# Performance work log

Measured on AMD Instinct MI355X. Metric: run time of the kernel, lower is better.

## Reference

```python
import jax, jax.numpy as jnp
import numpy as np

D_IN = 1024
D_OUT = 1024
N_HEADS = 16
HEAD_DIM = D_IN // N_HEADS      # 64
HEAD_DIM_V = D_OUT // N_HEADS   # 64


def setup_inputs() -> dict:
    key = jax.random.key(0)
    ks = jax.random.split(key, 7)
    s = 0.02
    x = jax.random.normal(ks[0], (4, 2048, D_IN), dtype=jnp.float32)
    Wq = jax.random.normal(ks[1], (D_IN, D_IN), dtype=jnp.float32) * s
    bq = jnp.zeros((D_IN,), dtype=jnp.float32)
    Wk = jax.random.normal(ks[2], (D_IN, D_IN), dtype=jnp.float32) * s
    bk = jnp.zeros((D_IN,), dtype=jnp.float32)
    Wv = jax.random.normal(ks[3], (D_IN, D_OUT), dtype=jnp.float32) * s
    bv = jnp.zeros((D_OUT,), dtype=jnp.float32)
    return {"x": x, "Wq": Wq, "bq": bq, "Wk": Wk, "bk": bk, "Wv": Wv, "bv": bv}


def reference(x, Wq, bq, Wk, bk, Wv, bv):
    B, S, _ = x.shape
    scale = jnp.sqrt(jnp.asarray(HEAD_DIM, dtype=jnp.float32))
    # projections -> [B, S, H, Dh] -> [B, H, S, Dh]
    q = (x @ Wq + bq).reshape(B, S, N_HEADS, HEAD_DIM).transpose(0, 2, 1, 3)
    k = (x @ Wk + bk).reshape(B, S, N_HEADS, HEAD_DIM).transpose(0, 2, 1, 3)
    v = (x @ Wv + bv).reshape(B, S, N_HEADS, HEAD_DIM_V).transpose(0, 2, 1, 3)
    # [B, H, S, S] attention scores (naive full materialization, as in source)
    scores = jnp.einsum("bhsd,bhtd->bhst", q, k) / scale
    weights = jax.nn.softmax(scores, axis=-1)
    out = jnp.einsum("bhst,bhtd->bhsd", weights, v)
    # [B, H, S, Dv] -> [B, S, H*Dv]  (out_projection NOT applied in source forward)
    return out.transpose(0, 2, 1, 3).reshape(B, S, N_HEADS * HEAD_DIM_V)
```

## Files before the change

### kernel.cpp

```cpp
#include <hip/hip_runtime.h>

#define B_  4
#define S_  2048
#define D_  1024
#define H_  16
#define DH_ 64
#define M_  (B_ * S_)

typedef __attribute__((ext_vector_type(8))) short short8;
typedef __attribute__((ext_vector_type(4))) float floatx4;

__device__ __forceinline__ unsigned short f2bf(float f) {
    union { float f; unsigned int i; } v; v.f = f;
    unsigned int r = v.i + 0x7fffu + ((v.i >> 16) & 1u);
    return (unsigned short)(r >> 16);
}
__device__ __forceinline__ unsigned int pk_trunc(float a, float b) {
#if __has_builtin(__builtin_amdgcn_perm)
    return __builtin_amdgcn_perm(__float_as_uint(b), __float_as_uint(a), 0x07060302u);
#else
    return (__float_as_uint(a) >> 16) | (__float_as_uint(b) & 0xffff0000u);
#endif
}

#if __has_builtin(__builtin_amdgcn_exp2f)
#define EXP2(x) __builtin_amdgcn_exp2f(x)
#else
#define EXP2(x) __expf(0.6931471805599453f * (x))
#endif

typedef const __attribute__((address_space(1))) unsigned int* gas_ptr;
typedef __attribute__((address_space(3))) unsigned int* las_ptr;
__device__ __forceinline__ void async_cp16(const void* g, void* l) {
    __builtin_amdgcn_global_load_lds((gas_ptr)g, (las_ptr)l, 16, 0, 0);
}

#define VMC3 asm volatile("s_waitcnt vmcnt(3)" ::: "memory")
#define VMC0 asm volatile("s_waitcnt vmcnt(0)" ::: "memory")

__global__ __launch_bounds__(256) void cast_fused_kernel(
    const float* __restrict__ x, unsigned short* __restrict__ Ax,
    const float* __restrict__ W0, const float* __restrict__ W1,
    const float* __restrict__ W2,
    unsigned short* __restrict__ T0, unsigned short* __restrict__ T1,
    unsigned short* __restrict__ T2)
{
    const int bid = blockIdx.x;
    const int t = threadIdx.x;
    if (bid < 8192) {
        int i4 = bid * 256 + t;
        float4 v = reinterpret_cast<const float4*>(x)[i4];
        ushort4 o;
        o.x = f2bf(v.x); o.y = f2bf(v.y); o.z = f2bf(v.z); o.w = f2bf(v.w);
        reinterpret_cast<ushort4*>(Ax)[i4] = o;
        return;
    }
    const int idx = bid - 8192;
    const int z   = idx >> 8;
    const int rem = idx & 255;
    const float* W = z == 0 ? W0 : (z == 1 ? W1 : W2);
    unsigned short* Wt = z == 0 ? T0 : (z == 1 ? T1 : T2);

    __shared__ unsigned short T[64][72];
    const int k0 = (rem & 15) * 64, n0 = (rem >> 4) * 64;

    #pragma unroll
    for (int p = 0; p < 4; ++p) {
        int kr = p * 16 + (t >> 4);
        int nc = (t & 15) * 4;
        float4 v = *reinterpret_cast<const float4*>(W + (size_t)(k0 + kr) * D_ + n0 + nc);
        T[nc + 0][kr] = f2bf(v.x);
        T[nc + 1][kr] = f2bf(v.y);
        T[nc + 2][kr] = f2bf(v.z);
        T[nc + 3][kr] = f2bf(v.w);
    }
    __syncthreads();

    const int nl = t >> 2, kc = (t & 3) * 16;
    size_t base = (size_t)(n0 + nl) * D_ + k0 + kc;
    *reinterpret_cast<short8*>(Wt + base)     = *reinterpret_cast<const short8*>(&T[nl][kc]);
    *reinterpret_cast<short8*>(Wt + base + 8) = *reinterpret_cast<const short8*>(&T[nl][kc + 8]);
}

__global__ __launch_bounds__(512) void gemm_qkv_mfma(
    const unsigned short* __restrict__ Ax,
    const unsigned short* __restrict__ Wt,
    const float* __restrict__ bq, const float* __restrict__ bk,
    const float* __restrict__ bv,
    unsigned short* __restrict__ Q,
    unsigned short* __restrict__ Vtg)
{
    __shared__ unsigned short lds[49152];

    const int tid  = threadIdx.x;
    const int lane = tid & 63;
    const int w    = tid >> 6;
    const int wm   = w >> 2;
    const int wn   = w & 3;
    const int l15  = lane & 15, quad = lane >> 4;

    const int pl   = tid >> 3;
    const int sl   = tid & 7;
    const int xx   = sl ^ (pl & 7);
    const int sro  = pl * 2 + (xx >> 2);
    const int sc   = (xx & 3) * 8;
    const int ldst = tid * 8;
    const int fb = (l15 >> 1) * 64 + ((((l15 & 1) << 2) | quad) ^ (l15 >> 1)) * 8;

    const int id  = blockIdx.x;
    const int g   = (id & 7) * 96 + (id >> 3);
    const int nb  = g >> 6;
    const int mb  = g & 63;
    const int m0  = mb * 128;
    const int n0g = nb * 256;
    const int mat = nb >> 2;
    const int n0m = (nb & 3) * 256;
    const float* bias = mat == 0 ? bq : (mat == 1 ? bk : bv);

    #define ASTG(kcol, reg) \
        async_cp16(Ax + (size_t)(m0 + sro) * 1024 + (kcol) + sc, lds + (reg) + ldst)
    #define BSTG(kcol, reg) do { \
        async_cp16(Wt + (size_t)(n0g + sro) * 1024 + (kcol) + sc,       lds + (reg) + ldst); \
        async_cp16(Wt + (size_t)(n0g + 128 + sro) * 1024 + (kcol) + sc, lds + (reg) + 4096 + ldst); \
    } while (0)

    floatx4 acc[4][4] = {};

    ASTG(0, 0);      BSTG(0, 8192);
    ASTG(32, 4096);  BSTG(32, 16384);
    ASTG(64, 24576); BSTG(64, 32768);
    VMC3;
    __builtin_amdgcn_s_barrier();

    #define PH(bufS, ksub, STAGE_STMT, WAIT_STMT) do { \
        short8 af[4], bfr[4]; \
        _Pragma("unroll") \
        for (int i = 0; i < 4; ++i) \
            af[i] = *reinterpret_cast<const short8*>(lds + (bufS) + (ksub) * 4096 + wm * 2048 + i * 512 + fb); \
        _Pragma("unroll") \
        for (int j = 0; j < 4; ++j) \
            bfr[j] = *reinterpret_cast<const short8*>(lds + (bufS) + 8192 + (ksub) * 8192 + wn * 2048 + j * 512 + fb); \
        STAGE_STMT; \
        __builtin_amdgcn_s_barrier(); \
        asm volatile("s_waitcnt lgkmcnt(0)" ::: "memory"); \
        __builtin_amdgcn_sched_barrier(0); \
        __builtin_amdgcn_s_setprio(1); \
        _Pragma("unroll") \
        for (int i = 0; i < 4; ++i) \
            _Pragma("unroll") \
            for (int j = 0; j < 4; ++j) \
                acc[i][j] = __builtin_amdgcn_mfma_f32_16x16x32_bf16(af[i], bfr[j], acc[i][j], 0, 0, 0); \
        __builtin_amdgcn_s_setprio(0); \
        WAIT_STMT; \
        __builtin_amdgcn_s_barrier(); \
    } while (0)

    #pragma unroll 1
    for (int it = 0; it < 8; ++it) {
        const bool nl = (it < 7);
        const int  kA = (2 * it + 1) * 64;
        const int  kB = kA + 64;
        const int  kC = kA + 128;
        PH(0,     0, { ASTG(kA + 32, 28672); BSTG(kA + 32, 40960); }, );
        PH(0,     1, if (nl) { ASTG(kB, 0); BSTG(kB, 8192); }, { if (nl) VMC3; else VMC0; });
        PH(24576, 0, if (nl) { ASTG(kB + 32, 4096); BSTG(kB + 32, 16384); }, );
        PH(24576, 1, if (nl) { ASTG(kC, 24576); BSTG(kC, 32768); }, { if (nl) VMC3; });
    }

    float bb[4];
    #pragma unroll
    for (int j = 0; j < 4; ++j) bb[j] = bias[n0m + wn * 64 + j * 16 + l15];

    if (mat == 2) {
        const int bI    = m0 >> 11;
        #pragma unroll
        for (int i = 0; i < 4; ++i) {
            int srow = (m0 & 2047) + wm * 64 + i * 16 + quad * 4;
            #pragma unroll
            for (int j = 0; j < 4; ++j) {
                int col = n0m + wn * 64 + j * 16 + l15;
                ushort4 o;
                o.x = f2bf(acc[i][j][0] + bb[j]);
                o.y = f2bf(acc[i][j][1] + bb[j]);
                o.z = f2bf(acc[i][j][2] + bb[j]);
                o.w = f2bf(acc[i][j][3] + bb[j]);
                *reinterpret_cast<ushort4*>(Vtg + (size_t)(bI * 1024 + col) * S_ + srow) = o;
            }
        }
    } else {
        unsigned short* C = Q + (size_t)mat * M_ * D_;
        const float scq = (mat == 0) ? 0.18033688011112042f : 1.0f;
        #pragma unroll
        for (int i = 0; i < 4; ++i)
            #pragma unroll
            for (int r = 0; r < 4; ++r) {
                int row = m0 + wm * 64 + i * 16 + quad * 4 + r;
                #pragma unroll
                for (int j = 0; j < 4; ++j)
                    C[(size_t)row * D_ + n0m + wn * 64 + j * 16 + l15] = f2bf((acc[i][j][r] + bb[j]) * scq);
            }
    }
}

#define KT_   64
#define NT_   (S_ / KT_)
#define PITCH 72

__global__ __launch_bounds__(256, 4) void attn_mfma(
    const unsigned short* __restrict__ Qg,
    const unsigned short* __restrict__ Kg,
    const unsigned short* __restrict__ Vtg,
    float* __restrict__ out)
{
    __shared__ unsigned short Ks[KT_ * PITCH];
    __shared__ unsigned short Vt[DH_ * PITCH];

    const int tid  = threadIdx.x;
    const int wq   = tid >> 6;
    const int lane = tid & 63;
    const int l15  = lane & 15;
    const int quad = lane >> 4;

    const int id  = blockIdx.x;
    const int bh  = (id & 7) * 8 + ((id >> 3) & 7);
    const int qt  = id >> 6;
    const int b   = bh >> 4;
    const int colbase = (bh & 15) * DH_;
    const int rowQ0 = b * S_ + qt * 128;

    short8 qf[2][2];
    #pragma unroll
    for (int g = 0; g < 2; ++g) {
        int qrow = rowQ0 + wq * 32 + g * 16 + l15;
        qf[g][0] = *reinterpret_cast<const short8*>(Qg + (size_t)qrow * D_ + colbase + quad * 8);
        qf[g][1] = *reinterpret_cast<const short8*>(Qg + (size_t)qrow * D_ + colbase + 32 + quad * 8);
    }

    short8 vones;
    #pragma unroll
    for (int i = 0; i < 8; ++i) vones[i] = (short)0x3F80;

    floatx4 Oacc[2][4] = {};
    floatx4 Lacc[2] = {};

    const int srow = tid >> 3;
    const int sc8  = (tid & 7) * 8;
    const int vc  = sc8 >> 4;
    const int vqk = (sc8 >> 2) & 3;
    const int vk0 = ((vc & 1) << 2) + ((vc >> 1) << 5) + (vqk << 3);

    const unsigned short* Kbase = Kg + (size_t)(b * S_) * D_ + colbase;
    const unsigned short* Vbase = Vtg + (size_t)(bh * 64) * S_;

    short8 kpre[2], vpre[2];
    #pragma unroll
    for (int p = 0; p < 2; ++p) {
        kpre[p] = *reinterpret_cast<const short8*>(Kbase + (size_t)(p * 32 + srow) * D_ + sc8);
        vpre[p] = *reinterpret_cast<const short8*>(Vbase + (size_t)(p * 32 + srow) * S_ + sc8);
    }

    for (int kt = 0; kt < NT_; ++kt) {
        __syncthreads();
        #pragma unroll
        for (int p = 0; p < 2; ++p) {
            *reinterpret_cast<short8*>(&Ks[(p * 32 + srow) * PITCH + sc8]) = kpre[p];
            uint4 u = __builtin_bit_cast(uint4, vpre[p]);
            uint2 lo, hi;
            lo.x = u.x; lo.y = u.y; hi.x = u.z; hi.y = u.w;
            *reinterpret_cast<uint2*>(&Vt[(p * 32 + srow) * PITCH + vk0])     = lo;
            *reinterpret_cast<uint2*>(&Vt[(p * 32 + srow) * PITCH + vk0 + 8]) = hi;
        }
        __syncthreads();
        if (kt + 1 < NT_) {
            int off = (kt + 1) * KT_;
            #pragma unroll
            for (int p = 0; p < 2; ++p) {
                kpre[p] = *reinterpret_cast<const short8*>(Kbase + (size_t)(off + p * 32 + srow) * D_ + sc8);
                vpre[p] = *reinterpret_cast<const short8*>(Vbase + (size_t)(p * 32 + srow) * S_ + off + sc8);
            }
        }

        #pragma unroll
        for (int half = 0; half < 2; ++half) {
            floatx4 s_[2][2];
            __builtin_amdgcn_s_setprio(1);
            #pragma unroll
            for (int ci = 0; ci < 2; ++ci) {
                int c = half * 2 + ci;
                short8 kf0 = *reinterpret_cast<const short8*>(&Ks[(c * 16 + l15) * PITCH + quad * 8]);
                short8 kf1 = *reinterpret_cast<const short8*>(&Ks[(c * 16 + l15) * PITCH + 32 + quad * 8]);
                #pragma unroll
                for (int g = 0; g < 2; ++g) {
                    floatx4 a = {0.f, 0.f, 0.f, 0.f};
                    a = __builtin_amdgcn_mfma_f32_16x16x32_bf16(kf0, qf[g][0], a, 0, 0, 0);
                    a = __builtin_amdgcn_mfma_f32_16x16x32_bf16(kf1, qf[g][1], a, 0, 0, 0);
                    s_[g][ci] = a;
                }
            }
            __builtin_amdgcn_s_setprio(0);
            short8 pa[2];
            #pragma unroll
            for (int g = 0; g < 2; ++g) {
                float p00 = EXP2(s_[g][0][0]), p01 = EXP2(s_[g][0][1]);
                float p02 = EXP2(s_[g][0][2]), p03 = EXP2(s_[g][0][3]);
                float p10 = EXP2(s_[g][1][0]), p11 = EXP2(s_[g][1][1]);
                float p12 = EXP2(s_[g][1][2]), p13 = EXP2(s_[g][1][3]);
                uint4 pu;
                pu.x = pk_trunc(p00, p01);
                pu.y = pk_trunc(p02, p03);
                pu.z = pk_trunc(p10, p11);
                pu.w = pk_trunc(p12, p13);
                pa[g] = __builtin_bit_cast(short8, pu);
            }
            __builtin_amdgcn_s_setprio(1);
            #pragma unroll
            for (int g = 0; g < 2; ++g)
                Lacc[g] = __builtin_amdgcn_mfma_f32_16x16x32_bf16(pa[g], vones, Lacc[g], 0, 0, 0);
            #pragma unroll
            for (int d = 0; d < 4; ++d) {
                short8 vf = *reinterpret_cast<const short8*>(
                    &Vt[(d * 16 + l15) * PITCH + half * 32 + quad * 8]);
                #pragma unroll
                for (int g = 0; g < 2; ++g)
                    Oacc[g][d] = __builtin_amdgcn_mfma_f32_16x16x32_bf16(pa[g], vf, Oacc[g][d], 0, 0, 0);
            }
            __builtin_amdgcn_s_setprio(0);
        }
    }

    #pragma unroll
    for (int g = 0; g < 2; ++g) {
        int orow = rowQ0 + wq * 32 + g * 16 + quad * 4;
        #pragma unroll
        for (int r = 0; r < 4; ++r) {
            float inv = 1.f / Lacc[g][r];
            #pragma unroll
            for (int d = 0; d < 4; ++d)
                out[(size_t)(orow + r) * D_ + colbase + d * 16 + l15] = Oacc[g][d][r] * inv;
        }
    }
}

extern "C" void kernel_launch(void* const* d_in, const int* in_sizes, int n_in,
                              void* d_out, int out_size, void* d_ws, size_t ws_size,
                              hipStream_t stream) {
    const float* x  = (const float*)d_in[0];
    const float* Wq = (const float*)d_in[1];
    const float* bq = (const float*)d_in[2];
    const float* Wk = (const float*)d_in[3];
    const float* bk = (const float*)d_in[4];
    const float* Wv = (const float*)d_in[5];
    const float* bv = (const float*)d_in[6];
    float* out = (float*)d_out;

    unsigned short* Q   = (unsigned short*)d_ws;
    unsigned short* K   = Q + (size_t)M_ * D_;
    unsigned short* Vtg = K + (size_t)M_ * D_;
    unsigned short* Ax  = Vtg + (size_t)M_ * D_;
    unsigned short* Wtq = Ax + (size_t)M_ * D_;
    unsigned short* Wtk = Wtq + (size_t)D_ * D_;
    unsigned short* Wtv = Wtk + (size_t)D_ * D_;

    cast_fused_kernel<<<8192 + 768, 256, 0, stream>>>(x, Ax, Wq, Wk, Wv, Wtq, Wtk, Wtv);

    gemm_qkv_mfma<<<768, 512, 0, stream>>>(Ax, Wtq, bq, bk, bv, Q, Vtg);

    attn_mfma<<<1024, 256, 0, stream>>>(Q, K, Vtg, out);
}
```

Before: 232.1 us.

## Double-buffer K/V shared-memory tiles in attention kernel

Splits the K and V shared-memory tiles into two buffers so the next tile is written to LDS while the current one is consumed, with global loads prefetched two tiles ahead. This cuts the two barriers per iteration to one and lets LDS stores overlap the MFMA compute. It doubles LDS use per block (about 36 KB), which may lower occupancy under launch_bounds(256,4), and it keeps the prefetch registers live across the whole loop body.

```diff
diff --git a/kernel.cpp b/kernel.cpp
--- a/kernel.cpp
+++ b/kernel.cpp
@@ -212,8 +212,8 @@
     const unsigned short* __restrict__ Vtg,
     float* __restrict__ out)
 {
-    __shared__ unsigned short Ks[KT_ * PITCH];
-    __shared__ unsigned short Vt[DH_ * PITCH];
+    __shared__ unsigned short Ks[2][KT_ * PITCH];
+    __shared__ unsigned short Vt[2][DH_ * PITCH];
 
     const int tid  = threadIdx.x;
     const int wq   = tid >> 6;
@@ -258,25 +258,46 @@
         kpre[p] = *reinterpret_cast<const short8*>(Kbase + (size_t)(p * 32 + srow) * D_ + sc8);
         vpre[p] = *reinterpret_cast<const short8*>(Vbase + (size_t)(p * 32 + srow) * S_ + sc8);
     }
+    #pragma unroll
+    for (int p = 0; p < 2; ++p) {
+        *reinterpret_cast<short8*>(&Ks[0][(p * 32 + srow) * PITCH + sc8]) = kpre[p];
+        uint4 u = __builtin_bit_cast(uint4, vpre[p]);
+        uint2 lo, hi;
+        lo.x = u.x; lo.y = u.y; hi.x = u.z; hi.y = u.w;
+        *reinterpret_cast<uint2*>(&Vt[0][(p * 32 + srow) * PITCH + vk0])     = lo;
+        *reinterpret_cast<uint2*>(&Vt[0][(p * 32 + srow) * PITCH + vk0 + 8]) = hi;
+    }
+    #pragma unroll
+    for (int p = 0; p < 2; ++p) {
+        kpre[p] = *reinterpret_cast<const short8*>(Kbase + (size_t)(KT_ + p * 32 + srow) * D_ + sc8);
+        vpre[p] = *reinterpret_cast<const short8*>(Vbase + (size_t)(p * 32 + srow) * S_ + KT_ + sc8);
+    }
+    __syncthreads();
 
     for (int kt = 0; kt < NT_; ++kt) {
-        __syncthreads();
-        #pragma unroll
-        for (int p = 0; p < 2; ++p) {
-            *reinterpret_cast<short8*>(&Ks[(p * 32 + srow) * PITCH + sc8]) = kpre[p];
-            uint4 u = __builtin_bit_cast(uint4, vpre[p]);
-            uint2 lo, hi;
-            lo.x = u.x; lo.y = u.y; hi.x = u.z; hi.y = u.w;
-            *reinterpret_cast<uint2*>(&Vt[(p * 32 + srow) * PITCH + vk0])     = lo;
-            *reinterpret_cast<uint2*>(&Vt[(p * 32 + srow) * PITCH + vk0 + 8]) = hi;
-        }
-        __syncthreads();
+        const int cur = kt & 1;
+        const unsigned short* Kc = &Ks[cur][0];
+        const unsigned short* Vc = &Vt[cur][0];
+
         if (kt + 1 < NT_) {
-            int off = (kt + 1) * KT_;
+            unsigned short* Kn = &Ks[cur ^ 1][0];
+            unsigned short* Vn = &Vt[cur ^ 1][0];
             #pragma unroll
             for (int p = 0; p < 2; ++p) {
-                kpre[p] = *reinterpret_cast<const short8*>(Kbase + (size_t)(off + p * 32 + srow) * D_ + sc8);
-                vpre[p] = *reinterpret_cast<const short8*>(Vbase + (size_t)(p * 32 + srow) * S_ + off + sc8);
+                *reinterpret_cast<short8*>(&Kn[(p * 32 + srow) * PITCH + sc8]) = kpre[p];
+                uint4 u = __builtin_bit_cast(uint4, vpre[p]);
+                uint2 lo, hi;
+                lo.x = u.x; lo.y = u.y; hi.x = u.z; hi.y = u.w;
+                *reinterpret_cast<uint2*>(&Vn[(p * 32 + srow) * PITCH + vk0])     = lo;
+                *reinterpret_cast<uint2*>(&Vn[(p * 32 + srow) * PITCH + vk0 + 8]) = hi;
+            }
+            if (kt + 2 < NT_) {
+                int off = (kt + 2) * KT_;
+                #pragma unroll
+                for (int p = 0; p < 2; ++p) {
+                    kpre[p] = *reinterpret_cast<const short8*>(Kbase + (size_t)(off + p * 32 + srow) * D_ + sc8);
+                    vpre[p] = *reinterpret_cast<const short8*>(Vbase + (size_t)(p * 32 + srow) * S_ + off + sc8);
+                }
             }
         }
 
@@ -287,8 +308,8 @@
             #pragma unroll
             for (int ci = 0; ci < 2; ++ci) {
                 int c = half * 2 + ci;
-                short8 kf0 = *reinterpret_cast<const short8*>(&Ks[(c * 16 + l15) * PITCH + quad * 8]);
-                short8 kf1 = *reinterpret_cast<const short8*>(&Ks[(c * 16 + l15) * PITCH + 32 + quad * 8]);
+                short8 kf0 = *reinterpret_cast<const short8*>(&Kc[(c * 16 + l15) * PITCH + quad * 8]);
+                short8 kf1 = *reinterpret_cast<const short8*>(&Kc[(c * 16 + l15) * PITCH + 32 + quad * 8]);
                 #pragma unroll
                 for (int g = 0; g < 2; ++g) {
                     floatx4 a = {0.f, 0.f, 0.f, 0.f};
@@ -319,13 +340,14 @@
             #pragma unroll
             for (int d = 0; d < 4; ++d) {
                 short8 vf = *reinterpret_cast<const short8*>(
-                    &Vt[(d * 16 + l15) * PITCH + half * 32 + quad * 8]);
+                    &Vc[(d * 16 + l15) * PITCH + half * 32 + quad * 8]);
                 #pragma unroll
                 for (int g = 0; g < 2; ++g)
                     Oacc[g][d] = __builtin_amdgcn_mfma_f32_16x16x32_bf16(pa[g], vf, Oacc[g][d], 0, 0, 0);
             }
             __builtin_amdgcn_s_setprio(0);
         }
+        __syncthreads();
     }
 
     #pragma unroll
```

Result: slower. 241.1 us (+3.9%).
